# Optimization experiments

Measured on AMD Instinct MI355X. Metric: run time of the kernel, lower is better.

## Reference

```python
import jax, jax.numpy as jnp
import numpy as np

NUM_USERS = 100000
EMB = 128
B = 4096
K = 64


def setup_inputs() -> dict:
    key = jax.random.key(0)
    ks = jax.random.split(key, 8)
    s = 1.0 / np.sqrt(EMB)
    return {
        "node_idx": jax.random.randint(ks[0], (B,), 0, NUM_USERS),
        "neigh_idx": jax.random.randint(ks[1], (B, K), 0, NUM_USERS),
        "neigh_len": jax.random.randint(ks[2], (B,), 0, K + 1),
        "u2e_visual": jax.random.normal(ks[3], (NUM_USERS, EMB), jnp.float32),
        "u2e_text": jax.random.normal(ks[4], (NUM_USERS, EMB), jnp.float32),
        "att_w1": jax.random.normal(ks[5], (2 * EMB, EMB), jnp.float32) * s,
        "att_b1": jnp.zeros((EMB,), jnp.float32),
        "att_w2": jax.random.normal(ks[6], (EMB, EMB), jnp.float32) * s,
        "att_b2": jnp.zeros((EMB,), jnp.float32),
        "att_w3": jax.random.normal(ks[7], (EMB, 1), jnp.float32) * s,
        "att_b3": jnp.zeros((1,), jnp.float32),
    }


def _attend_aggregate(node_rep, neigh_feat, mask, w1, b1, w2, b2, w3, b3):
    # node_rep [B,D], neigh_feat [B,K,D], mask [B,K] bool
    Bn, Kn, D = neigh_feat.shape
    node_b = jnp.broadcast_to(node_rep[:, None, :], (Bn, Kn, D))
    x = jnp.concatenate([neigh_feat, node_b], axis=-1)        # [B,K,2D]
    h = jax.nn.relu(x @ w1 + b1)                              # [B,K,D]
    h = jax.nn.relu(h @ w2 + b2)                              # [B,K,D]
    scores = (h @ w3 + b3)[..., 0]                            # [B,K]
    scores = jnp.where(mask, scores, jnp.float32(-1e30))
    att = jax.nn.softmax(scores, axis=-1)                     # [B,K]
    agg = jnp.einsum('bk,bkd->bd', att, neigh_feat)           # weighted sum
    has_neigh = mask.any(axis=-1, keepdims=True)              # empty list -> self rep
    return jnp.where(has_neigh, agg, node_rep)


def reference(node_idx, neigh_idx, neigh_len, u2e_visual, u2e_text,
              att_w1, att_b1, att_w2, att_b2, att_w3, att_b3):
    mask = jnp.arange(K)[None, :] < neigh_len[:, None]        # [B,K]
    u_v = u2e_visual[node_idx]                                # [B,D]
    u_t = u2e_text[node_idx]                                  # [B,D]
    n_v = u2e_visual[neigh_idx]                               # [B,K,D]
    n_t = u2e_text[neigh_idx]                                 # [B,K,D]
    v_agg = _attend_aggregate(u_v, n_v, mask, att_w1, att_b1, att_w2, att_b2, att_w3, att_b3)
    t_agg = _attend_aggregate(u_t, n_t, mask, att_w1, att_b1, att_w2, att_b2, att_w3, att_b3)
    # (u_v_embed_matrix, u_t_embed_matrix, v_embed_matrix, t_embed_matrix), stacked
    return jnp.stack([u_v, u_t, v_agg, t_agg], axis=0)        # [4,B,D]
```

## Files before the change

kernel.cpp:

```cpp
#include <hip/hip_runtime.h>
#include <math.h>

#define NB 4096
#define KN 64
#define DIM 128
#define HP 136

typedef __bf16 bf16;
typedef bf16 bf16x8 __attribute__((ext_vector_type(8)));
typedef bf16 bf16x4 __attribute__((ext_vector_type(4)));
typedef float f32x4 __attribute__((ext_vector_type(4)));

__global__ void prep_weights(const float* __restrict__ w1,
                             const float* __restrict__ w2,
                             bf16* __restrict__ w1T,
                             bf16* __restrict__ w2T) {
    int t = blockIdx.x * 256 + threadIdx.x;
    if (t < 128 * 256) {
        int j = t >> 8, i = t & 255;
        w1T[t] = (bf16)w1[i * 128 + j];
    } else {
        int t2 = t - 128 * 256;
        int j2 = t2 >> 7, j1 = t2 & 127;
        w2T[t2] = (bf16)w2[j1 * 128 + j2];
    }
}

__global__ __launch_bounds__(256, 4) void graphsage_mfma(
    const int* __restrict__ node_idx,
    const int* __restrict__ neigh_idx,
    const int* __restrict__ neigh_len,
    const float* __restrict__ emb_v,
    const float* __restrict__ emb_t,
    const bf16* __restrict__ w1T,
    const float* __restrict__ b1,
    const bf16* __restrict__ w2T,
    const float* __restrict__ b2,
    const float* __restrict__ w3,
    float* __restrict__ out)
{
    __shared__ bf16  n_lds[KN][HP];
    __shared__ bf16  h1_lds[KN][HP];
    __shared__ float u_lds[2][DIM];
    __shared__ float uq_lds[2][DIM];
    __shared__ float scratch[4][DIM];
    __shared__ float att_lds[KN];
    __shared__ int   ni_lds[KN];

    const int b   = blockIdx.x;
    const int tid = threadIdx.x;
    const int nd  = node_idx[b];
    const int len = neigh_len[b];

    const int wv = tid >> 6;
    const int ll = tid & 15;
    const int lh = (tid >> 4) & 3;

    float uvv = 0.f, uvt = 0.f;
    if (tid < DIM) {
        uvv = emb_v[(size_t)nd * DIM + tid];
        uvt = emb_t[(size_t)nd * DIM + tid];
        out[((size_t)0 * NB + b) * DIM + tid] = uvv;
        out[((size_t)1 * NB + b) * DIM + tid] = uvt;
    }
    if (len == 0) {
        if (tid < DIM) {
            out[((size_t)2 * NB + b) * DIM + tid] = uvv;
            out[((size_t)3 * NB + b) * DIM + tid] = uvt;
        }
        return;
    }
    if (tid < DIM) { u_lds[0][tid] = uvv; u_lds[1][tid] = uvt; }
    if (tid < KN) ni_lds[tid] = neigh_idx[b * KN + tid];
    __syncthreads();

    {
        int j = tid & 127, h = tid >> 7;
        const bf16* wb = w1T + (size_t)j * 256 + DIM + h * 64;
        const float* usv = &u_lds[0][h * 64];
        const float* ust = &u_lds[1][h * 64];
        float av = 0.f, at = 0.f;
        #pragma unroll
        for (int i = 0; i < 64; i += 8) {
            bf16x8 w = *(const bf16x8*)(wb + i);
            #pragma unroll
            for (int q = 0; q < 8; ++q) {
                float wf = (float)w[q];
                av = fmaf(usv[i + q], wf, av);
                at = fmaf(ust[i + q], wf, at);
            }
        }
        scratch[h][j] = av;
        scratch[2 + h][j] = at;
    }
    __syncthreads();
    {
        int j = tid & 127, mm = tid >> 7;
        uq_lds[mm][j] = scratch[mm * 2][j] + scratch[mm * 2 + 1][j] + b1[j];
    }
    __syncthreads();

    const int nkt = (len + 15) >> 4;
    const int lim = nkt * 16;

    for (int m = 0; m < 2; ++m) {
        const float* __restrict__ emb = m ? emb_t : emb_v;

        for (int c = tid; c < lim * 16; c += 256) {
            int r = c >> 4, c8 = c & 15;
            bf16x8 v;
            if (r < len) {
                const float* src = emb + (size_t)ni_lds[r] * DIM + c8 * 8;
                float4 f0 = ((const float4*)src)[0];
                float4 f1 = ((const float4*)src)[1];
                v[0] = (bf16)f0.x; v[1] = (bf16)f0.y; v[2] = (bf16)f0.z; v[3] = (bf16)f0.w;
                v[4] = (bf16)f1.x; v[5] = (bf16)f1.y; v[6] = (bf16)f1.z; v[7] = (bf16)f1.w;
            } else {
                #pragma unroll
                for (int q = 0; q < 8; ++q) v[q] = (bf16)0.f;
            }
            *(bf16x8*)&n_lds[r][c8 * 8] = v;
        }
        __syncthreads();

        {
            bf16x8 af[2][4];
            #pragma unroll
            for (int jt = 0; jt < 2; ++jt)
                #pragma unroll
                for (int ks = 0; ks < 4; ++ks)
                    af[jt][ks] = *(const bf16x8*)(w1T + (size_t)(wv * 32 + jt * 16 + ll) * 256 + ks * 32 + lh * 8);

            f32x4 zero4 = {0.f, 0.f, 0.f, 0.f};
            f32x4 acc[2][4];
            #pragma unroll
            for (int kt = 0; kt < 4; ++kt) { acc[0][kt] = zero4; acc[1][kt] = zero4; }

            #pragma unroll
            for (int kt = 0; kt < 4; ++kt) {
                if (kt < nkt) {
                    #pragma unroll
                    for (int ks = 0; ks < 4; ++ks) {
                        bf16x8 bfr = *(const bf16x8*)&n_lds[kt * 16 + ll][ks * 32 + lh * 8];
                        acc[0][kt] = __builtin_amdgcn_mfma_f32_16x16x32_bf16(af[0][ks], bfr, acc[0][kt], 0, 0, 0);
                        acc[1][kt] = __builtin_amdgcn_mfma_f32_16x16x32_bf16(af[1][ks], bfr, acc[1][kt], 0, 0, 0);
                    }
                }
            }
            #pragma unroll
            for (int jt = 0; jt < 2; ++jt) {
                float4 uq4 = *(const float4*)&uq_lds[m][wv * 32 + jt * 16 + lh * 4];
                float uqa[4] = {uq4.x, uq4.y, uq4.z, uq4.w};
                #pragma unroll
                for (int kt = 0; kt < 4; ++kt) {
                    if (kt < nkt) {
                        bf16x4 hv;
                        #pragma unroll
                        for (int r = 0; r < 4; ++r)
                            hv[r] = (bf16)fmaxf(acc[jt][kt][r] + uqa[r], 0.f);
                        *(bf16x4*)&h1_lds[kt * 16 + ll][wv * 32 + jt * 16 + lh * 4] = hv;
                    }
                }
            }
        }
        __syncthreads();

        {
            bf16x8 af2[2][4];
            #pragma unroll
            for (int mtl = 0; mtl < 2; ++mtl)
                #pragma unroll
                for (int ks = 0; ks < 4; ++ks)
                    af2[mtl][ks] = *(const bf16x8*)(w2T + (size_t)(wv * 32 + mtl * 16 + ll) * 128 + ks * 32 + lh * 8);

            f32x4 zero4 = {0.f, 0.f, 0.f, 0.f};
            f32x4 acc2[2][4];
            #pragma unroll
            for (int ntk = 0; ntk < 4; ++ntk) { acc2[0][ntk] = zero4; acc2[1][ntk] = zero4; }

            #pragma unroll
            for (int ntk = 0; ntk < 4; ++ntk) {
                if (ntk < nkt) {
                    #pragma unroll
                    for (int ks = 0; ks < 4; ++ks) {
                        bf16x8 bfr = *(const bf16x8*)&h1_lds[ntk * 16 + ll][ks * 32 + lh * 8];
                        acc2[0][ntk] = __builtin_amdgcn_mfma_f32_16x16x32_bf16(af2[0][ks], bfr, acc2[0][ntk], 0, 0, 0);
                        acc2[1][ntk] = __builtin_amdgcn_mfma_f32_16x16x32_bf16(af2[1][ks], bfr, acc2[1][ntk], 0, 0, 0);
                    }
                }
            }

            float4 w3a = *(const float4*)(w3 + wv * 32 + lh * 4);
            float4 w3b = *(const float4*)(w3 + wv * 32 + 16 + lh * 4);
            float4 b2a = *(const float4*)(b2 + wv * 32 + lh * 4);
            float4 b2b = *(const float4*)(b2 + wv * 32 + 16 + lh * 4);
            float w3arr[8] = {w3a.x, w3a.y, w3a.z, w3a.w, w3b.x, w3b.y, w3b.z, w3b.w};
            float b2arr[8] = {b2a.x, b2a.y, b2a.z, b2a.w, b2b.x, b2b.y, b2b.z, b2b.w};
            #pragma unroll
            for (int ntk = 0; ntk < 4; ++ntk) {
                if (ntk < nkt) {
                    float s = 0.f;
                    #pragma unroll
                    for (int r = 0; r < 4; ++r) {
                        s = fmaf(fmaxf(acc2[0][ntk][r] + b2arr[r],     0.f), w3arr[r],     s);
                        s = fmaf(fmaxf(acc2[1][ntk][r] + b2arr[4 + r], 0.f), w3arr[4 + r], s);
                    }
                    s += __shfl_xor(s, 16);
                    s += __shfl_xor(s, 32);
                    if (lh == 0) scratch[wv][ntk * 16 + ll] = s;
                }
            }
        }
        __syncthreads();

        if (tid < KN) {
            float s = scratch[0][tid] + scratch[1][tid] + scratch[2][tid] + scratch[3][tid];
            float sv = (tid < len) ? s : -INFINITY;
            float mx = sv;
            #pragma unroll
            for (int off = 1; off < 64; off <<= 1) mx = fmaxf(mx, __shfl_xor(mx, off));
            float e = (tid < len) ? __expf(sv - mx) : 0.f;
            float sum = e;
            #pragma unroll
            for (int off = 1; off < 64; off <<= 1) sum += __shfl_xor(sum, off);
            att_lds[tid] = e / sum;
        }
        __syncthreads();

        {
            int jg = tid & 31, ks = tid >> 5;
            int j0 = jg * 4;
            float ax = 0.f, ay = 0.f, az = 0.f, aw = 0.f;
            int kb = ks * 8, ke = min(len, kb + 8);
            for (int k = kb; k < ke; ++k) {
                float av = att_lds[k];
                bf16x4 nv = *(const bf16x4*)&n_lds[k][j0];
                ax = fmaf(av, (float)nv[0], ax);
                ay = fmaf(av, (float)nv[1], ay);
                az = fmaf(av, (float)nv[2], az);
                aw = fmaf(av, (float)nv[3], aw);
            }
            ax += __shfl_xor(ax, 32);
            ay += __shfl_xor(ay, 32);
            az += __shfl_xor(az, 32);
            aw += __shfl_xor(aw, 32);
            if ((tid & 63) < 32) {
                float4 v4 = {ax, ay, az, aw};
                *(float4*)&scratch[wv][j0] = v4;
            }
        }
        __syncthreads();
        if (tid < DIM)
            out[((size_t)(2 + m) * NB + b) * DIM + tid] =
                scratch[0][tid] + scratch[1][tid] + scratch[2][tid] + scratch[3][tid];
        __syncthreads();
    }
}

extern "C" void kernel_launch(void* const* d_in, const int* in_sizes, int n_in,
                              void* d_out, int out_size, void* d_ws, size_t ws_size,
                              hipStream_t stream) {
    const int*   node_idx  = (const int*)d_in[0];
    const int*   neigh_idx = (const int*)d_in[1];
    const int*   neigh_len = (const int*)d_in[2];
    const float* emb_v     = (const float*)d_in[3];
    const float* emb_t     = (const float*)d_in[4];
    const float* w1        = (const float*)d_in[5];
    const float* b1        = (const float*)d_in[6];
    const float* w2        = (const float*)d_in[7];
    const float* b2        = (const float*)d_in[8];
    const float* w3        = (const float*)d_in[9];
    float* out = (float*)d_out;

    bf16* w1T = (bf16*)d_ws;
    bf16* w2T = (bf16*)d_ws + 128 * 256;

    hipLaunchKernelGGL(prep_weights, dim3(192), dim3(256), 0, stream, w1, w2, w1T, w2T);
    hipLaunchKernelGGL(graphsage_mfma, dim3(NB), dim3(256), 0, stream,
                       node_idx, neigh_idx, neigh_len, emb_v, emb_t,
                       w1T, b1, w2T, b2, w3, out);
}
```

Measured before the change: 96.73 us.

## Split modalities across grid, gather neighbors directly into MFMA fragments

The main kernel now launches one block per (node, modality) instead of looping over both modalities in one block, which doubles parallelism. Neighbor rows are loaded straight from global memory into registers as MFMA B-fragments, so the LDS staging buffer is gone. The node-side projection now runs on MFMA, and the weighted sum rereads the fp32 embeddings from global memory. Self-embedding copies and the empty-neighbor fallback move into the weight-prep kernel. The cost is gathering each neighbor row twice and running more, smaller blocks.

```diff
diff --git a/kernel.cpp b/kernel.cpp
--- a/kernel.cpp
+++ b/kernel.cpp
@@ -4,26 +4,44 @@
 #define NB 4096
 #define KN 64
 #define DIM 128
-#define HP 136
+#define HP 132
 
 typedef __bf16 bf16;
 typedef bf16 bf16x8 __attribute__((ext_vector_type(8)));
 typedef bf16 bf16x4 __attribute__((ext_vector_type(4)));
 typedef float f32x4 __attribute__((ext_vector_type(4)));
 
-__global__ void prep_weights(const float* __restrict__ w1,
-                             const float* __restrict__ w2,
-                             bf16* __restrict__ w1T,
-                             bf16* __restrict__ w2T) {
-    int t = blockIdx.x * 256 + threadIdx.x;
-    if (t < 128 * 256) {
-        int j = t >> 8, i = t & 255;
-        w1T[t] = (bf16)w1[i * 128 + j];
-    } else {
-        int t2 = t - 128 * 256;
-        int j2 = t2 >> 7, j1 = t2 & 127;
-        w2T[t2] = (bf16)w2[j1 * 128 + j2];
-    }
+__global__ void prep_and_copy(const float* __restrict__ w1,
+                              const float* __restrict__ w2,
+                              bf16* __restrict__ w1T,
+                              bf16* __restrict__ w2T,
+                              const int* __restrict__ node_idx,
+                              const int* __restrict__ neigh_len,
+                              const float* __restrict__ emb_v,
+                              const float* __restrict__ emb_t,
+                              float* __restrict__ out) {
+    int blk = blockIdx.x;
+    if (blk < 192) {
+        int t = blk * 256 + threadIdx.x;
+        if (t < 128 * 256) {
+            int j = t >> 8, i = t & 255;
+            w1T[t] = (bf16)w1[i * 128 + j];
+        } else {
+            int t2 = t - 128 * 256;
+            int j2 = t2 >> 7, j1 = t2 & 127;
+            w2T[t2] = (bf16)w2[j1 * 128 + j2];
+        }
+        return;
+    }
+    int b = blk - 192;
+    int tid = threadIdx.x;
+    int m = tid >> 7, j = tid & 127;
+    int nd = node_idx[b], len = neigh_len[b];
+    const float* emb = m ? emb_t : emb_v;
+    float uv = emb[(size_t)nd * DIM + j];
+    out[((size_t)m * NB + b) * DIM + j] = uv;
+    if (len == 0)
+        out[((size_t)(2 + m) * NB + b) * DIM + j] = uv;
 }
 
 __global__ __launch_bounds__(256, 4) void graphsage_mfma(
@@ -39,222 +57,187 @@
     const float* __restrict__ w3,
     float* __restrict__ out)
 {
-    __shared__ bf16  n_lds[KN][HP];
     __shared__ bf16  h1_lds[KN][HP];
-    __shared__ float u_lds[2][DIM];
-    __shared__ float uq_lds[2][DIM];
     __shared__ float scratch[4][DIM];
     __shared__ float att_lds[KN];
     __shared__ int   ni_lds[KN];
+    __shared__ bf16  u_bf[DIM];
 
     const int b   = blockIdx.x;
+    const int m   = blockIdx.y;
     const int tid = threadIdx.x;
-    const int nd  = node_idx[b];
     const int len = neigh_len[b];
+    if (len == 0) return;
+
+    const float* __restrict__ emb = m ? emb_t : emb_v;
 
     const int wv = tid >> 6;
     const int ll = tid & 15;
     const int lh = (tid >> 4) & 3;
 
-    float uvv = 0.f, uvt = 0.f;
-    if (tid < DIM) {
-        uvv = emb_v[(size_t)nd * DIM + tid];
-        uvt = emb_t[(size_t)nd * DIM + tid];
-        out[((size_t)0 * NB + b) * DIM + tid] = uvv;
-        out[((size_t)1 * NB + b) * DIM + tid] = uvt;
-    }
-    if (len == 0) {
-        if (tid < DIM) {
-            out[((size_t)2 * NB + b) * DIM + tid] = uvv;
-            out[((size_t)3 * NB + b) * DIM + tid] = uvt;
-        }
-        return;
-    }
-    if (tid < DIM) { u_lds[0][tid] = uvv; u_lds[1][tid] = uvt; }
     if (tid < KN) ni_lds[tid] = neigh_idx[b * KN + tid];
-    __syncthreads();
+    if (tid < DIM) u_bf[tid] = (bf16)emb[(size_t)node_idx[b] * DIM + tid];
+    __syncthreads();
+
+    const int nkt = (len + 15) >> 4;
+    const f32x4 zero4 = {0.f, 0.f, 0.f, 0.f};
+    const float4 zf4 = {0.f, 0.f, 0.f, 0.f};
 
     {
-        int j = tid & 127, h = tid >> 7;
-        const bf16* wb = w1T + (size_t)j * 256 + DIM + h * 64;
-        const float* usv = &u_lds[0][h * 64];
-        const float* ust = &u_lds[1][h * 64];
-        float av = 0.f, at = 0.f;
-        #pragma unroll
-        for (int i = 0; i < 64; i += 8) {
-            bf16x8 w = *(const bf16x8*)(wb + i);
+        f32x4 accu[2] = {zero4, zero4};
+        {
             #pragma unroll
-            for (int q = 0; q < 8; ++q) {
-                float wf = (float)w[q];
-                av = fmaf(usv[i + q], wf, av);
-                at = fmaf(ust[i + q], wf, at);
-            }
-        }
-        scratch[h][j] = av;
-        scratch[2 + h][j] = at;
-    }
-    __syncthreads();
+            for (int ks = 0; ks < 4; ++ks) {
+                bf16x8 bu = *(const bf16x8*)&u_bf[ks * 32 + lh * 8];
+                bf16x8 a0 = *(const bf16x8*)(w1T + (size_t)(wv * 32 + ll) * 256 + 128 + ks * 32 + lh * 8);
+                bf16x8 a1 = *(const bf16x8*)(w1T + (size_t)(wv * 32 + 16 + ll) * 256 + 128 + ks * 32 + lh * 8);
+                accu[0] = __builtin_amdgcn_mfma_f32_16x16x32_bf16(a0, bu, accu[0], 0, 0, 0);
+                accu[1] = __builtin_amdgcn_mfma_f32_16x16x32_bf16(a1, bu, accu[1], 0, 0, 0);
+            }
+        }
+        float4 b1q0 = *(const float4*)(b1 + wv * 32 + lh * 4);
+        float4 b1q1 = *(const float4*)(b1 + wv * 32 + 16 + lh * 4);
+        float bq0[4] = {b1q0.x, b1q0.y, b1q0.z, b1q0.w};
+        float bq1[4] = {b1q1.x, b1q1.y, b1q1.z, b1q1.w};
+
+        bf16x8 af[2][4];
+        #pragma unroll
+        for (int jt = 0; jt < 2; ++jt)
+            #pragma unroll
+            for (int ks = 0; ks < 4; ++ks)
+                af[jt][ks] = *(const bf16x8*)(w1T + (size_t)(wv * 32 + jt * 16 + ll) * 256 + ks * 32 + lh * 8);
+
+        #pragma unroll
+        for (int kt = 0; kt < 4; ++kt) {
+            if (kt < nkt) {
+                int row = kt * 16 + ll;
+                bool vld = row < len;
+                const float* src = emb + (size_t)ni_lds[vld ? row : 0] * DIM;
+                bf16x8 bfr[4];
+                #pragma unroll
+                for (int ks = 0; ks < 4; ++ks) {
+                    float4 f0 = zf4, f1 = zf4;
+                    if (vld) {
+                        f0 = ((const float4*)(src + ks * 32 + lh * 8))[0];
+                        f1 = ((const float4*)(src + ks * 32 + lh * 8))[1];
+                    }
+                    bf16x8 v;
+                    v[0] = (bf16)f0.x; v[1] = (bf16)f0.y; v[2] = (bf16)f0.z; v[3] = (bf16)f0.w;
+                    v[4] = (bf16)f1.x; v[5] = (bf16)f1.y; v[6] = (bf16)f1.z; v[7] = (bf16)f1.w;
+                    bfr[ks] = v;
+                }
+                f32x4 a0 = zero4, a1 = zero4;
+                #pragma unroll
+                for (int ks = 0; ks < 4; ++ks) {
+                    a0 = __builtin_amdgcn_mfma_f32_16x16x32_bf16(af[0][ks], bfr[ks], a0, 0, 0, 0);
+                    a1 = __builtin_amdgcn_mfma_f32_16x16x32_bf16(af[1][ks], bfr[ks], a1, 0, 0, 0);
+                }
+                bf16x4 h0, h1v;
+                #pragma unroll
+                for (int r = 0; r < 4; ++r) {
+                    h0[r]  = (bf16)fmaxf(a0[r] + accu[0][r] + bq0[r], 0.f);
+                    h1v[r] = (bf16)fmaxf(a1[r] + accu[1][r] + bq1[r], 0.f);
+                }
+                *(bf16x4*)&h1_lds[row][wv * 32 + lh * 4]      = h0;
+                *(bf16x4*)&h1_lds[row][wv * 32 + 16 + lh * 4] = h1v;
+            }
+        }
+    }
+    __syncthreads();
+
     {
-        int j = tid & 127, mm = tid >> 7;
-        uq_lds[mm][j] = scratch[mm * 2][j] + scratch[mm * 2 + 1][j] + b1[j];
-    }
-    __syncthreads();
-
-    const int nkt = (len + 15) >> 4;
-    const int lim = nkt * 16;
-
-    for (int m = 0; m < 2; ++m) {
-        const float* __restrict__ emb = m ? emb_t : emb_v;
-
-        for (int c = tid; c < lim * 16; c += 256) {
-            int r = c >> 4, c8 = c & 15;
-            bf16x8 v;
-            if (r < len) {
-                const float* src = emb + (size_t)ni_lds[r] * DIM + c8 * 8;
-                float4 f0 = ((const float4*)src)[0];
-                float4 f1 = ((const float4*)src)[1];
-                v[0] = (bf16)f0.x; v[1] = (bf16)f0.y; v[2] = (bf16)f0.z; v[3] = (bf16)f0.w;
-                v[4] = (bf16)f1.x; v[5] = (bf16)f1.y; v[6] = (bf16)f1.z; v[7] = (bf16)f1.w;
-            } else {
-                #pragma unroll
-                for (int q = 0; q < 8; ++q) v[q] = (bf16)0.f;
-            }
-            *(bf16x8*)&n_lds[r][c8 * 8] = v;
-        }
-        __syncthreads();
-
-        {
-            bf16x8 af[2][4];
+        bf16x8 af2[2][4];
+        #pragma unroll
+        for (int mtl = 0; mtl < 2; ++mtl)
             #pragma unroll
-            for (int jt = 0; jt < 2; ++jt)
+            for (int ks = 0; ks < 4; ++ks)
+                af2[mtl][ks] = *(const bf16x8*)(w2T + (size_t)(wv * 32 + mtl * 16 + ll) * 128 + ks * 32 + lh * 8);
+
+        float4 w3a = *(const float4*)(w3 + wv * 32 + lh * 4);
+        float4 w3b = *(const float4*)(w3 + wv * 32 + 16 + lh * 4);
+        float4 b2a = *(const float4*)(b2 + wv * 32 + lh * 4);
+        float4 b2b = *(const float4*)(b2 + wv * 32 + 16 + lh * 4);
+        float w3q0[4] = {w3a.x, w3a.y, w3a.z, w3a.w};
+        float w3q1[4] = {w3b.x, w3b.y, w3b.z, w3b.w};
+        float b2q0[4] = {b2a.x, b2a.y, b2a.z, b2a.w};
+        float b2q1[4] = {b2b.x, b2b.y, b2b.z, b2b.w};
+
+        #pragma unroll
+        for (int ntk = 0; ntk < 4; ++ntk) {
+            if (ntk < nkt) {
+                bf16x8 bfr[4];
                 #pragma unroll
                 for (int ks = 0; ks < 4; ++ks)
-                    af[jt][ks] = *(const bf16x8*)(w1T + (size_t)(wv * 32 + jt * 16 + ll) * 256 + ks * 32 + lh * 8);
-
-            f32x4 zero4 = {0.f, 0.f, 0.f, 0.f};
-            f32x4 acc[2][4];
-            #pragma unroll
-            for (int kt = 0; kt < 4; ++kt) { acc[0][kt] = zero4; acc[1][kt] = zero4; }
-
-            #pragma unroll
-            for (int kt = 0; kt < 4; ++kt) {
-                if (kt < nkt) {
-                    #pragma unroll
-                    for (int ks = 0; ks < 4; ++ks) {
-                        bf16x8 bfr = *(const bf16x8*)&n_lds[kt * 16 + ll][ks * 32 + lh * 8];
-                        acc[0][kt] = __builtin_amdgcn_mfma_f32_16x16x32_bf16(af[0][ks], bfr, acc[0][kt], 0, 0, 0);
-                        acc[1][kt] = __builtin_amdgcn_mfma_f32_16x16x32_bf16(af[1][ks], bfr, acc[1][kt], 0, 0, 0);
-                    }
-                }
-            }
-            #pragma unroll
-            for (int jt = 0; jt < 2; ++jt) {
-                float4 uq4 = *(const float4*)&uq_lds[m][wv * 32 + jt * 16 + lh * 4];
-                float uqa[4] = {uq4.x, uq4.y, uq4.z, uq4.w};
-                #pragma unroll
-                for (int kt = 0; kt < 4; ++kt) {
-                    if (kt < nkt) {
-                        bf16x4 hv;
-                        #pragma unroll
-                        for (int r = 0; r < 4; ++r)
-                            hv[r] = (bf16)fmaxf(acc[jt][kt][r] + uqa[r], 0.f);
-                        *(bf16x4*)&h1_lds[kt * 16 + ll][wv * 32 + jt * 16 + lh * 4] = hv;
-                    }
-                }
-            }
-        }
-        __syncthreads();
-
-        {
-            bf16x8 af2[2][4];
-            #pragma unroll
-            for (int mtl = 0; mtl < 2; ++mtl)
-                #pragma unroll
-                for (int ks = 0; ks < 4; ++ks)
-                    af2[mtl][ks] = *(const bf16x8*)(w2T + (size_t)(wv * 32 + mtl * 16 + ll) * 128 + ks * 32 + lh * 8);
-
-            f32x4 zero4 = {0.f, 0.f, 0.f, 0.f};
-            f32x4 acc2[2][4];
-            #pragma unroll
-            for (int ntk = 0; ntk < 4; ++ntk) { acc2[0][ntk] = zero4; acc2[1][ntk] = zero4; }
-
-            #pragma unroll
-            for (int ntk = 0; ntk < 4; ++ntk) {
-                if (ntk < nkt) {
-                    #pragma unroll
-                    for (int ks = 0; ks < 4; ++ks) {
-                        bf16x8 bfr = *(const bf16x8*)&h1_lds[ntk * 16 + ll][ks * 32 + lh * 8];
-                        acc2[0][ntk] = __builtin_amdgcn_mfma_f32_16x16x32_bf16(af2[0][ks], bfr, acc2[0][ntk], 0, 0, 0);
-                        acc2[1][ntk] = __builtin_amdgcn_mfma_f32_16x16x32_bf16(af2[1][ks], bfr, acc2[1][ntk], 0, 0, 0);
-                    }
-                }
-            }
-
-            float4 w3a = *(const float4*)(w3 + wv * 32 + lh * 4);
-            float4 w3b = *(const float4*)(w3 + wv * 32 + 16 + lh * 4);
-            float4 b2a = *(const float4*)(b2 + wv * 32 + lh * 4);
-            float4 b2b = *(const float4*)(b2 + wv * 32 + 16 + lh * 4);
-            float w3arr[8] = {w3a.x, w3a.y, w3a.z, w3a.w, w3b.x, w3b.y, w3b.z, w3b.w};
-            float b2arr[8] = {b2a.x, b2a.y, b2a.z, b2a.w, b2b.x, b2b.y, b2b.z, b2b.w};
-            #pragma unroll
-            for (int ntk = 0; ntk < 4; ++ntk) {
-                if (ntk < nkt) {
-                    float s = 0.f;
-                    #pragma unroll
-                    for (int r = 0; r < 4; ++r) {
-                        s = fmaf(fmaxf(acc2[0][ntk][r] + b2arr[r],     0.f), w3arr[r],     s);
-                        s = fmaf(fmaxf(acc2[1][ntk][r] + b2arr[4 + r], 0.f), w3arr[4 + r], s);
-                    }
-                    s += __shfl_xor(s, 16);
-                    s += __shfl_xor(s, 32);
-                    if (lh == 0) scratch[wv][ntk * 16 + ll] = s;
-                }
-            }
-        }
-        __syncthreads();
-
-        if (tid < KN) {
-            float s = scratch[0][tid] + scratch[1][tid] + scratch[2][tid] + scratch[3][tid];
-            float sv = (tid < len) ? s : -INFINITY;
-            float mx = sv;
-            #pragma unroll
-            for (int off = 1; off < 64; off <<= 1) mx = fmaxf(mx, __shfl_xor(mx, off));
-            float e = (tid < len) ? __expf(sv - mx) : 0.f;
-            float sum = e;
-            #pragma unroll
-            for (int off = 1; off < 64; off <<= 1) sum += __shfl_xor(sum, off);
-            att_lds[tid] = e / sum;
-        }
-        __syncthreads();
-
-        {
-            int jg = tid & 31, ks = tid >> 5;
-            int j0 = jg * 4;
-            float ax = 0.f, ay = 0.f, az = 0.f, aw = 0.f;
-            int kb = ks * 8, ke = min(len, kb + 8);
-            for (int k = kb; k < ke; ++k) {
-                float av = att_lds[k];
-                bf16x4 nv = *(const bf16x4*)&n_lds[k][j0];
-                ax = fmaf(av, (float)nv[0], ax);
-                ay = fmaf(av, (float)nv[1], ay);
-                az = fmaf(av, (float)nv[2], az);
-                aw = fmaf(av, (float)nv[3], aw);
-            }
-            ax += __shfl_xor(ax, 32);
-            ay += __shfl_xor(ay, 32);
-            az += __shfl_xor(az, 32);
-            aw += __shfl_xor(aw, 32);
-            if ((tid & 63) < 32) {
-                float4 v4 = {ax, ay, az, aw};
-                *(float4*)&scratch[wv][j0] = v4;
-            }
-        }
-        __syncthreads();
-        if (tid < DIM)
-            out[((size_t)(2 + m) * NB + b) * DIM + tid] =
-                scratch[0][tid] + scratch[1][tid] + scratch[2][tid] + scratch[3][tid];
-        __syncthreads();
-    }
+                    bfr[ks] = *(const bf16x8*)&h1_lds[ntk * 16 + ll][ks * 32 + lh * 8];
+                f32x4 c0 = zero4, c1 = zero4;
+                #pragma unroll
+                for (int ks = 0; ks < 4; ++ks) {
+                    c0 = __builtin_amdgcn_mfma_f32_16x16x32_bf16(af2[0][ks], bfr[ks], c0, 0, 0, 0);
+                    c1 = __builtin_amdgcn_mfma_f32_16x16x32_bf16(af2[1][ks], bfr[ks], c1, 0, 0, 0);
+                }
+                float s = 0.f;
+                #pragma unroll
+                for (int r = 0; r < 4; ++r) {
+                    s = fmaf(fmaxf(c0[r] + b2q0[r], 0.f), w3q0[r], s);
+                    s = fmaf(fmaxf(c1[r] + b2q1[r], 0.f), w3q1[r], s);
+                }
+                s += __shfl_xor(s, 16);
+                s += __shfl_xor(s, 32);
+                if (lh == 0) scratch[wv][ntk * 16 + ll] = s;
+            }
+        }
+    }
+    __syncthreads();
+
+    const int sslice = tid >> 5;
+    const int j0 = (tid & 31) * 4;
+    float4 nv[8];
+    #pragma unroll
+    for (int q = 0; q < 8; ++q) {
+        int k = sslice + 8 * q;
+        nv[q] = (k < len) ? *(const float4*)(emb + (size_t)ni_lds[k] * DIM + j0) : zf4;
+    }
+
+    if (tid < KN) {
+        float s = scratch[0][tid] + scratch[1][tid] + scratch[2][tid] + scratch[3][tid];
+        float sv = (tid < len) ? s : -INFINITY;
+        float mx = sv;
+        #pragma unroll
+        for (int off = 1; off < 64; off <<= 1) mx = fmaxf(mx, __shfl_xor(mx, off));
+        float e = (tid < len) ? __expf(sv - mx) : 0.f;
+        float sum = e;
+        #pragma unroll
+        for (int off = 1; off < 64; off <<= 1) sum += __shfl_xor(sum, off);
+        att_lds[tid] = e / sum;
+    }
+    __syncthreads();
+
+    {
+        float ax = 0.f, ay = 0.f, az = 0.f, aw = 0.f;
+        #pragma unroll
+        for (int q = 0; q < 8; ++q) {
+            int k = sslice + 8 * q;
+            if (k < len) {
+                float a = att_lds[k];
+                ax = fmaf(a, nv[q].x, ax);
+                ay = fmaf(a, nv[q].y, ay);
+                az = fmaf(a, nv[q].z, az);
+                aw = fmaf(a, nv[q].w, aw);
+            }
+        }
+        ax += __shfl_xor(ax, 32);
+        ay += __shfl_xor(ay, 32);
+        az += __shfl_xor(az, 32);
+        aw += __shfl_xor(aw, 32);
+        if ((tid & 63) < 32) {
+            float4 v4 = {ax, ay, az, aw};
+            *(float4*)&scratch[wv][j0] = v4;
+        }
+    }
+    __syncthreads();
+    if (tid < DIM)
+        out[((size_t)(2 + m) * NB + b) * DIM + tid] =
+            scratch[0][tid] + scratch[1][tid] + scratch[2][tid] + scratch[3][tid];
 }
 
 extern "C" void kernel_launch(void* const* d_in, const int* in_sizes, int n_in,
@@ -275,8 +258,9 @@
     bf16* w1T = (bf16*)d_ws;
     bf16* w2T = (bf16*)d_ws + 128 * 256;
 
-    hipLaunchKernelGGL(prep_weights, dim3(192), dim3(256), 0, stream, w1, w2, w1T, w2T);
-    hipLaunchKernelGGL(graphsage_mfma, dim3(NB), dim3(256), 0, stream,
+    hipLaunchKernelGGL(prep_and_copy, dim3(192 + NB), dim3(256), 0, stream,
+                       w1, w2, w1T, w2T, node_idx, neigh_len, emb_v, emb_t, out);
+    hipLaunchKernelGGL(graphsage_mfma, dim3(NB, 2), dim3(256), 0, stream,
                        node_idx, neigh_idx, neigh_len, emb_v, emb_t,
                        w1T, b1, w2T, b2, w3, out);
 }
```

After: 190.7 us. +97.2%, slower.
